# Kernel tuning notes

Measured on AMD Instinct MI355X. Metric: run time of the kernel, lower is better.

Reference implementation:

```python
import jax, jax.numpy as jnp
import numpy as np

N = 50000        # number of nodes
E = 1600000      # number of (directed) edges, ~degree 32
D = 128          # latent_dim
L = 2            # num_layers
NEG_SLOPE = 0.01 # torch F.leaky_relu default


def setup_inputs() -> dict:
    key = jax.random.key(0)
    k1, k2, k3, k4 = jax.random.split(key, 4)
    h = jax.random.normal(k1, (N, D), dtype=jnp.float32)
    src = jax.random.randint(k2, (E,), 0, N, dtype=jnp.int32)
    dst = jax.random.randint(k3, (E,), 0, N, dtype=jnp.int32)
    # attn_fc per layer: Linear(2*D, 1, bias=False) -> weight vector of length 2*D
    att_w = jax.random.normal(k4, (L, 2 * D), dtype=jnp.float32) * 0.1
    return {"h": h, "src": src, "dst": dst, "att_w": att_w}


def _segment_softmax(e, seg, n):
    # numerically-stable softmax over edges grouped by destination node
    m = jax.ops.segment_max(e, seg, num_segments=n)      # [N]
    ex = jnp.exp(e - m[seg])                             # [E]
    s = jax.ops.segment_sum(ex, seg, num_segments=n)     # [N]
    return ex / s[seg]


def reference(h, src, dst, att_w):
    n, d = h.shape
    for l in range(att_w.shape[0]):
        w_src = att_w[l, :d]   # weight applied to edges.src['h']
        w_dst = att_w[l, d:]   # weight applied to edges.dst['h']
        # a = attn_fc(concat(h_src, h_dst)) = h_src @ w_src + h_dst @ w_dst
        a = h[src] @ w_src + h[dst] @ w_dst               # [E]
        e = jnp.where(a > 0, a, NEG_SLOPE * a)            # leaky_relu
        alpha = _segment_softmax(e, dst, n)               # edge_softmax by dst
        # update_all: m = h_src * e ; h_dst = sum(m)
        h = jax.ops.segment_sum(h[src] * alpha[:, None], dst, num_segments=n)
    return h
```

## Files before the change

### kernel.cpp

```cpp
#include <hip/hip_runtime.h>
#include <hip/hip_fp16.h>
#include <math.h>

#define NEG_SLOPE 0.01f
#define BKT_BITS 7
#define BKT_MASK 127
#define SBLOCKS  256
#define STPB     512


__global__ void bkhist_kernel(const int* __restrict__ dst, int* __restrict__ blockhist,
                              int E, int NB, int chunk) {
    extern __shared__ int lh[];
    for (int k = threadIdx.x; k < NB; k += blockDim.x) lh[k] = 0;
    __syncthreads();
    int b = blockIdx.x;
    int beg = b * chunk, end = min(E, beg + chunk);
    for (int e = beg + (int)threadIdx.x; e < end; e += blockDim.x)
        atomicAdd(&lh[dst[e] >> BKT_BITS], 1);
    __syncthreads();
    for (int k = threadIdx.x; k < NB; k += blockDim.x)
        blockhist[k * SBLOCKS + b] = lh[k];
}

__global__ void scan1_kernel(const int* __restrict__ in, int* __restrict__ local_excl,
                             int* __restrict__ partials, int n) {
    __shared__ int sm[1024];
    int i = blockIdx.x * 1024 + threadIdx.x;
    int x = (i < n) ? in[i] : 0;
    sm[threadIdx.x] = x;
    __syncthreads();
    for (int off = 1; off < 1024; off <<= 1) {
        int y = (threadIdx.x >= (unsigned)off) ? sm[threadIdx.x - off] : 0;
        __syncthreads();
        sm[threadIdx.x] += y;
        __syncthreads();
    }
    if (i < n) local_excl[i] = sm[threadIdx.x] - x;
    if (threadIdx.x == 1023) partials[blockIdx.x] = sm[1023];
}

__global__ void scan2_kernel(int* __restrict__ partials, int nchunks) {
    __shared__ int sm[1024];
    int x = (threadIdx.x < (unsigned)nchunks) ? partials[threadIdx.x] : 0;
    sm[threadIdx.x] = x;
    __syncthreads();
    for (int off = 1; off < 1024; off <<= 1) {
        int y = (threadIdx.x >= (unsigned)off) ? sm[threadIdx.x - off] : 0;
        __syncthreads();
        sm[threadIdx.x] += y;
        __syncthreads();
    }
    partials[threadIdx.x] = sm[threadIdx.x] - x;
    if (threadIdx.x == 1023) partials[1024] = sm[1023];
}

__device__ __forceinline__ int bh_at(const int* __restrict__ local_ex,
                                     const int* __restrict__ partials, int i) {
    return local_ex[i] + partials[i >> 10];
}

__global__ void bksplit_kernel(const int* __restrict__ src, const int* __restrict__ dst,
                               const int* __restrict__ local_ex, const int* __restrict__ partials,
                               unsigned* __restrict__ pairs,
                               int E, int NB, int chunk) {
    extern __shared__ int lm[];
    int* lbase = lm;
    int* lcnt  = lm + NB;
    int b = blockIdx.x;
    for (int k = threadIdx.x; k < NB; k += blockDim.x) {
        lbase[k] = bh_at(local_ex, partials, k * SBLOCKS + b);
        lcnt[k]  = 0;
    }
    __syncthreads();
    int beg = b * chunk, end = min(E, beg + chunk);
    for (int e = beg + (int)threadIdx.x; e < end; e += blockDim.x) {
        int d = dst[e];
        int k = d >> BKT_BITS;
        int pos = lbase[k] + atomicAdd(&lcnt[k], 1);
        pairs[pos] = ((unsigned)src[e] << BKT_BITS) | (unsigned)(d & BKT_MASK);
    }
}

__global__ void csr_build_kernel(const unsigned* __restrict__ pairs,
                                 const int* __restrict__ local_ex, const int* __restrict__ partials,
                                 int* __restrict__ row_ptr, int* __restrict__ csr_src,
                                 int E, int N, int NB) {
    __shared__ int ldeg[128];
    __shared__ int lscan[128];
    __shared__ int lpos[128];
    int k = blockIdx.x;
    int bbase = bh_at(local_ex, partials, k * SBLOCKS);
    int bend  = (k == NB - 1) ? E : bh_at(local_ex, partials, (k + 1) * SBLOCKS);
    if (threadIdx.x < 128) ldeg[threadIdx.x] = 0;
    __syncthreads();
    for (int i = bbase + (int)threadIdx.x; i < bend; i += blockDim.x)
        atomicAdd(&ldeg[pairs[i] & BKT_MASK], 1);
    __syncthreads();
    int x = (threadIdx.x < 128) ? ldeg[threadIdx.x] : 0;
    if (threadIdx.x < 128) lscan[threadIdx.x] = x;
    __syncthreads();
    for (int off = 1; off < 128; off <<= 1) {
        int y = 0;
        if (threadIdx.x < 128 && threadIdx.x >= (unsigned)off) y = lscan[threadIdx.x - off];
        __syncthreads();
        if (threadIdx.x < 128) lscan[threadIdx.x] += y;
        __syncthreads();
    }
    if (threadIdx.x < 128) {
        int excl = lscan[threadIdx.x] - x;
        int node = (k << BKT_BITS) + threadIdx.x;
        if (node < N) row_ptr[node] = bbase + excl;
        lpos[threadIdx.x] = excl;
    }
    if (k == NB - 1 && threadIdx.x == 0) row_ptr[N] = E;
    __syncthreads();
    for (int i = bbase + (int)threadIdx.x; i < bend; i += blockDim.x) {
        unsigned p = pairs[i];
        int pos = atomicAdd(&lpos[p & BKT_MASK], 1);
        csr_src[bbase + pos] = (int)(p >> BKT_BITS);
    }
}


__global__ void stconv_kernel(const float* __restrict__ h, const float* __restrict__ att_w_l,
                              float* __restrict__ s, float* __restrict__ t,
                              __half* __restrict__ h16, int n) {
    int gid  = blockIdx.x * blockDim.x + threadIdx.x;
    int wid  = gid >> 6;
    int lane = threadIdx.x & 63;
    int half = lane >> 5;
    int hl   = lane & 31;
    int v    = wid * 2 + half;
    if (v >= n) return;
    float4 hv = ((const float4*)(h + (size_t)v * 128))[hl];
    __half2 p01 = __floats2half2_rn(hv.x, hv.y);
    __half2 p23 = __floats2half2_rn(hv.z, hv.w);
    float2 packed;
    packed.x = *(const float*)&p01;
    packed.y = *(const float*)&p23;
    ((float2*)(h16 + (size_t)v * 128))[hl] = packed;
    float4 ws = ((const float4*)att_w_l)[hl];
    float4 wd = ((const float4*)(att_w_l + 128))[hl];
    float ps = hv.x * ws.x + hv.y * ws.y + hv.z * ws.z + hv.w * ws.w;
    float pt = hv.x * wd.x + hv.y * wd.y + hv.z * wd.z + hv.w * wd.w;
    for (int off = 16; off > 0; off >>= 1) {
        ps += __shfl_down(ps, off);
        pt += __shfl_down(pt, off);
    }
    if (hl == 0) { s[v] = ps; t[v] = pt; }
}

__device__ __forceinline__ void gath8(const __half* __restrict__ hin, int u, float w,
                                      int qlane, float acc[8]) {
    float4 r = ((const float4*)(hin + ((size_t)(unsigned)u << 7)))[qlane];
    const __half2* hp = (const __half2*)&r;
    #pragma unroll
    for (int d = 0; d < 4; ++d) {
        acc[2 * d]     = fmaf(__low2float(hp[d]),  w, acc[2 * d]);
        acc[2 * d + 1] = fmaf(__high2float(hp[d]), w, acc[2 * d + 1]);
    }
}

template<bool LAST>
__global__ __launch_bounds__(256, 8)
void agg_kernel(const __half* __restrict__ hin, const float* __restrict__ s,
                const float* __restrict__ t, const int* __restrict__ row_ptr,
                const int* __restrict__ csr_src,
                __half* __restrict__ hout16, float* __restrict__ outf,
                const float* __restrict__ att_w_next,
                float* __restrict__ s2, float* __restrict__ t2, int n) {
    int gid   = blockIdx.x * blockDim.x + threadIdx.x;
    int v     = gid >> 6;
    int lane  = threadIdx.x & 63;
    if (v >= n) return;
    int quad  = lane >> 4;
    int qlane = lane & 15;

    int beg = row_ptr[v];
    int end = row_ptr[v + 1];
    float tv = t[v];

    float acc[8] = {0.f, 0.f, 0.f, 0.f, 0.f, 0.f, 0.f, 0.f};
    float lsum_l = 0.f;

    for (int base = beg; base < end; base += 64) {
        int cnt = end - base;
        if (cnt > 64) cnt = 64;
        int idx = base + min(lane, cnt - 1);
        int u   = csr_src[idx];
        float a = s[u] + tv;
        float e = (a > 0.f) ? a : NEG_SLOPE * a;
        float wl = (lane < cnt) ? __expf(e) : 0.f;
        lsum_l += wl;
        int steps = (cnt + 3) >> 2;
        int k = 0;
        for (; k + 3 < steps; k += 4) {
            int sl0 = (k << 2) + quad;
            int   u0 = __shfl(u, sl0);       float w0 = __shfl(wl, sl0);
            int   u1 = __shfl(u, sl0 + 4);   float w1 = __shfl(wl, sl0 + 4);
            int   u2 = __shfl(u, sl0 + 8);   float w2 = __shfl(wl, sl0 + 8);
            int   u3 = __shfl(u, sl0 + 12);  float w3 = __shfl(wl, sl0 + 12);
            gath8(hin, u0, w0, qlane, acc);
            gath8(hin, u1, w1, qlane, acc);
            gath8(hin, u2, w2, qlane, acc);
            gath8(hin, u3, w3, qlane, acc);
        }
        for (; k < steps; ++k) {
            int sl = (k << 2) + quad;
            int   u0 = __shfl(u, sl);
            float w0 = __shfl(wl, sl);
            gath8(hin, u0, w0, qlane, acc);
        }
    }
    #pragma unroll
    for (int j = 0; j < 8; ++j) {
        acc[j] += __shfl_xor(acc[j], 16);
        acc[j] += __shfl_xor(acc[j], 32);
    }
    float lsum = lsum_l;
    for (int off = 32; off > 0; off >>= 1) lsum += __shfl_xor(lsum, off);
    float inv_l = (lsum > 0.f) ? (1.0f / lsum) : 0.f;
    #pragma unroll
    for (int j = 0; j < 8; ++j) acc[j] *= inv_l;

    if (LAST) {
        if (quad == 0) {
            float4* op = (float4*)(outf + (size_t)v * 128);
            op[2 * qlane]     = make_float4(acc[0], acc[1], acc[2], acc[3]);
            op[2 * qlane + 1] = make_float4(acc[4], acc[5], acc[6], acc[7]);
        }
    } else {
        if (quad == 0) {
            __half2 p0 = __floats2half2_rn(acc[0], acc[1]);
            __half2 p1 = __floats2half2_rn(acc[2], acc[3]);
            __half2 p2 = __floats2half2_rn(acc[4], acc[5]);
            __half2 p3 = __floats2half2_rn(acc[6], acc[7]);
            int4 pk;
            pk.x = *(const int*)&p0; pk.y = *(const int*)&p1;
            pk.z = *(const int*)&p2; pk.w = *(const int*)&p3;
            ((int4*)(hout16 + (size_t)v * 128))[qlane] = pk;
        }
        float4 ws0 = ((const float4*)att_w_next)[2 * qlane];
        float4 ws1 = ((const float4*)att_w_next)[2 * qlane + 1];
        float4 wd0 = ((const float4*)(att_w_next + 128))[2 * qlane];
        float4 wd1 = ((const float4*)(att_w_next + 128))[2 * qlane + 1];
        float ps = acc[0] * ws0.x + acc[1] * ws0.y + acc[2] * ws0.z + acc[3] * ws0.w
                 + acc[4] * ws1.x + acc[5] * ws1.y + acc[6] * ws1.z + acc[7] * ws1.w;
        float pt = acc[0] * wd0.x + acc[1] * wd0.y + acc[2] * wd0.z + acc[3] * wd0.w
                 + acc[4] * wd1.x + acc[5] * wd1.y + acc[6] * wd1.z + acc[7] * wd1.w;
        for (int off = 8; off > 0; off >>= 1) {
            ps += __shfl_down(ps, off);
            pt += __shfl_down(pt, off);
        }
        if (lane == 0) { s2[v] = ps; t2[v] = pt; }
    }
}


extern "C" void kernel_launch(void* const* d_in, const int* in_sizes, int n_in,
                              void* d_out, int out_size, void* d_ws, size_t ws_size,
                              hipStream_t stream) {
    const float* h0    = (const float*)d_in[0];
    const int*   src   = (const int*)d_in[1];
    const int*   dst   = (const int*)d_in[2];
    const float* att_w = (const float*)d_in[3];
    int N = in_sizes[0] / 128;
    int E = in_sizes[1];
    int L = in_sizes[3] / 256;
    float* out = (float*)d_out;

    int NB = (N + BKT_MASK) >> BKT_BITS;
    int n2 = NB * SBLOCKS;
    int chunk = (E + SBLOCKS - 1) / SBLOCKS;
    int nch2 = (n2 + 1023) / 1024;

    char* ws = (char*)d_ws;
    size_t off = 0;
    auto alloc = [&](size_t bytes) -> void* {
        void* p = ws + off;
        off = (off + bytes + 511) & ~(size_t)511;
        return p;
    };
    int*      row_ptr   = (int*)     alloc((size_t)(N + 1) * 4);
    int*      csr_src   = (int*)     alloc((size_t)E * 4);
    float*    s1        = (float*)   alloc((size_t)N * 4);
    float*    t1        = (float*)   alloc((size_t)N * 4);
    float*    s2        = (float*)   alloc((size_t)N * 4);
    float*    t2        = (float*)   alloc((size_t)N * 4);
    __half*   hA        = (__half*)  alloc((size_t)N * 128 * 2);
    __half*   hB        = (__half*)  alloc((size_t)N * 128 * 2);
    unsigned* pairs     = (unsigned*)alloc((size_t)E * 4);
    int*      blockhist = (int*)     alloc((size_t)n2 * 4);
    int*      local_ex  = (int*)     alloc((size_t)n2 * 4);
    int*      partials  = (int*)     alloc(1025 * 4);

    bkhist_kernel<<<SBLOCKS, STPB, NB * 4, stream>>>(dst, blockhist, E, NB, chunk);
    scan1_kernel<<<nch2, 1024, 0, stream>>>(blockhist, local_ex, partials, n2);
    scan2_kernel<<<1, 1024, 0, stream>>>(partials, nch2);
    bksplit_kernel<<<SBLOCKS, STPB, 2 * NB * 4, stream>>>(src, dst, local_ex, partials,
                                                          pairs, E, NB, chunk);
    csr_build_kernel<<<NB, 512, 0, stream>>>(pairs, local_ex, partials,
                                             row_ptr, csr_src, E, N, NB);

    const int tb = 256;
    int node_blocks = (N * 64 + tb - 1) / tb;
    int st_blocks   = ((N + 1) / 2 * 64 + tb - 1) / tb;

    stconv_kernel<<<st_blocks, tb, 0, stream>>>(h0, att_w, s1, t1, hA, N);

    __half* hin = hA;
    __half* hnx = hB;
    float *sc = s1, *tc = t1, *sn = s2, *tn = t2;
    for (int l = 0; l < L; ++l) {
        if (l == L - 1) {
            agg_kernel<true><<<node_blocks, tb, 0, stream>>>(
                hin, sc, tc, row_ptr, csr_src, nullptr, out, nullptr, nullptr, nullptr, N);
        } else {
            agg_kernel<false><<<node_blocks, tb, 0, stream>>>(
                hin, sc, tc, row_ptr, csr_src, hnx, nullptr,
                att_w + (size_t)(l + 1) * 256, sn, tn, N);
            __half* tmp = hin; hin = hnx; hnx = tmp;
            float* tf;
            tf = sc; sc = sn; sn = tf;
            tf = tc; tc = tn; tn = tf;
        }
    }
}
```

Baseline: 222.0 us.

## Replace bucketed two-pass CSR build with global atomic degree histogram and scatter

Swaps the bucket-sort CSR construction (per-block bucket histograms, bucket split into a pairs buffer, per-bucket local sort) for a direct scheme. It builds a global per-node degree histogram with atomics, scans it, then scatters each source into its slot with an atomicSub on the degree counter. The aggregation kernel now computes row offsets from the scan output and partials instead of a separate row_ptr array. This removes the pairs buffer and one pass over the edges, at the cost of heavy contention on global atomics and uncoalesced scattered writes. Neighbor order within a row also becomes nondeterministic, which changes floating-point summation order.

```diff
diff --git a/kernel.cpp b/kernel.cpp
--- a/kernel.cpp
+++ b/kernel.cpp
@@ -3,24 +3,12 @@
 #include <math.h>
 
 #define NEG_SLOPE 0.01f
-#define BKT_BITS 7
-#define BKT_MASK 127
-#define SBLOCKS  256
-#define STPB     512
-
-
-__global__ void bkhist_kernel(const int* __restrict__ dst, int* __restrict__ blockhist,
-                              int E, int NB, int chunk) {
-    extern __shared__ int lh[];
-    for (int k = threadIdx.x; k < NB; k += blockDim.x) lh[k] = 0;
-    __syncthreads();
-    int b = blockIdx.x;
-    int beg = b * chunk, end = min(E, beg + chunk);
-    for (int e = beg + (int)threadIdx.x; e < end; e += blockDim.x)
-        atomicAdd(&lh[dst[e] >> BKT_BITS], 1);
-    __syncthreads();
-    for (int k = threadIdx.x; k < NB; k += blockDim.x)
-        blockhist[k * SBLOCKS + b] = lh[k];
+
+
+__global__ void deghist_kernel(const int* __restrict__ dst, int* __restrict__ deg, int E) {
+    int stride = gridDim.x * blockDim.x;
+    for (int e = blockIdx.x * blockDim.x + threadIdx.x; e < E; e += stride)
+        atomicAdd(&deg[dst[e]], 1);
 }
 
 __global__ void scan1_kernel(const int* __restrict__ in, int* __restrict__ local_excl,
@@ -55,70 +43,15 @@
     if (threadIdx.x == 1023) partials[1024] = sm[1023];
 }
 
-__device__ __forceinline__ int bh_at(const int* __restrict__ local_ex,
-                                     const int* __restrict__ partials, int i) {
-    return local_ex[i] + partials[i >> 10];
-}
-
-__global__ void bksplit_kernel(const int* __restrict__ src, const int* __restrict__ dst,
-                               const int* __restrict__ local_ex, const int* __restrict__ partials,
-                               unsigned* __restrict__ pairs,
-                               int E, int NB, int chunk) {
-    extern __shared__ int lm[];
-    int* lbase = lm;
-    int* lcnt  = lm + NB;
-    int b = blockIdx.x;
-    for (int k = threadIdx.x; k < NB; k += blockDim.x) {
-        lbase[k] = bh_at(local_ex, partials, k * SBLOCKS + b);
-        lcnt[k]  = 0;
-    }
-    __syncthreads();
-    int beg = b * chunk, end = min(E, beg + chunk);
-    for (int e = beg + (int)threadIdx.x; e < end; e += blockDim.x) {
+__global__ void scatter_kernel(const int* __restrict__ src, const int* __restrict__ dst,
+                               const int* __restrict__ lex, const int* __restrict__ par,
+                               int* __restrict__ deg, int* __restrict__ csr_src, int E) {
+    int stride = gridDim.x * blockDim.x;
+    for (int e = blockIdx.x * blockDim.x + threadIdx.x; e < E; e += stride) {
         int d = dst[e];
-        int k = d >> BKT_BITS;
-        int pos = lbase[k] + atomicAdd(&lcnt[k], 1);
-        pairs[pos] = ((unsigned)src[e] << BKT_BITS) | (unsigned)(d & BKT_MASK);
-    }
-}
-
-__global__ void csr_build_kernel(const unsigned* __restrict__ pairs,
-                                 const int* __restrict__ local_ex, const int* __restrict__ partials,
-                                 int* __restrict__ row_ptr, int* __restrict__ csr_src,
-                                 int E, int N, int NB) {
-    __shared__ int ldeg[128];
-    __shared__ int lscan[128];
-    __shared__ int lpos[128];
-    int k = blockIdx.x;
-    int bbase = bh_at(local_ex, partials, k * SBLOCKS);
-    int bend  = (k == NB - 1) ? E : bh_at(local_ex, partials, (k + 1) * SBLOCKS);
-    if (threadIdx.x < 128) ldeg[threadIdx.x] = 0;
-    __syncthreads();
-    for (int i = bbase + (int)threadIdx.x; i < bend; i += blockDim.x)
-        atomicAdd(&ldeg[pairs[i] & BKT_MASK], 1);
-    __syncthreads();
-    int x = (threadIdx.x < 128) ? ldeg[threadIdx.x] : 0;
-    if (threadIdx.x < 128) lscan[threadIdx.x] = x;
-    __syncthreads();
-    for (int off = 1; off < 128; off <<= 1) {
-        int y = 0;
-        if (threadIdx.x < 128 && threadIdx.x >= (unsigned)off) y = lscan[threadIdx.x - off];
-        __syncthreads();
-        if (threadIdx.x < 128) lscan[threadIdx.x] += y;
-        __syncthreads();
-    }
-    if (threadIdx.x < 128) {
-        int excl = lscan[threadIdx.x] - x;
-        int node = (k << BKT_BITS) + threadIdx.x;
-        if (node < N) row_ptr[node] = bbase + excl;
-        lpos[threadIdx.x] = excl;
-    }
-    if (k == NB - 1 && threadIdx.x == 0) row_ptr[N] = E;
-    __syncthreads();
-    for (int i = bbase + (int)threadIdx.x; i < bend; i += blockDim.x) {
-        unsigned p = pairs[i];
-        int pos = atomicAdd(&lpos[p & BKT_MASK], 1);
-        csr_src[bbase + pos] = (int)(p >> BKT_BITS);
+        int slot = atomicSub(&deg[d], 1) - 1;
+        int base = lex[d] + par[d >> 10];
+        csr_src[base + slot] = src[e];
     }
 }
 
@@ -165,8 +98,8 @@
 template<bool LAST>
 __global__ __launch_bounds__(256, 8)
 void agg_kernel(const __half* __restrict__ hin, const float* __restrict__ s,
-                const float* __restrict__ t, const int* __restrict__ row_ptr,
-                const int* __restrict__ csr_src,
+                const float* __restrict__ t, const int* __restrict__ lex,
+                const int* __restrict__ par, const int* __restrict__ csr_src,
                 __half* __restrict__ hout16, float* __restrict__ outf,
                 const float* __restrict__ att_w_next,
                 float* __restrict__ s2, float* __restrict__ t2, int n) {
@@ -177,8 +110,8 @@
     int quad  = lane >> 4;
     int qlane = lane & 15;
 
-    int beg = row_ptr[v];
-    int end = row_ptr[v + 1];
+    int beg = lex[v]     + par[v >> 10];
+    int end = lex[v + 1] + par[(v + 1) >> 10];
     float tv = t[v];
 
     float acc[8] = {0.f, 0.f, 0.f, 0.f, 0.f, 0.f, 0.f, 0.f};
@@ -270,10 +203,8 @@
     int L = in_sizes[3] / 256;
     float* out = (float*)d_out;
 
-    int NB = (N + BKT_MASK) >> BKT_BITS;
-    int n2 = NB * SBLOCKS;
-    int chunk = (E + SBLOCKS - 1) / SBLOCKS;
-    int nch2 = (n2 + 1023) / 1024;
+    int n1 = N + 1;
+    int nch = (n1 + 1023) / 1024;
 
     char* ws = (char*)d_ws;
     size_t off = 0;
@@ -282,26 +213,22 @@
         off = (off + bytes + 511) & ~(size_t)511;
         return p;
     };
-    int*      row_ptr   = (int*)     alloc((size_t)(N + 1) * 4);
     int*      csr_src   = (int*)     alloc((size_t)E * 4);
+    int*      deg       = (int*)     alloc((size_t)n1 * 4);
+    int*      local_ex  = (int*)     alloc((size_t)n1 * 4);
+    int*      partials  = (int*)     alloc(1025 * 4);
     float*    s1        = (float*)   alloc((size_t)N * 4);
     float*    t1        = (float*)   alloc((size_t)N * 4);
     float*    s2        = (float*)   alloc((size_t)N * 4);
     float*    t2        = (float*)   alloc((size_t)N * 4);
     __half*   hA        = (__half*)  alloc((size_t)N * 128 * 2);
     __half*   hB        = (__half*)  alloc((size_t)N * 128 * 2);
-    unsigned* pairs     = (unsigned*)alloc((size_t)E * 4);
-    int*      blockhist = (int*)     alloc((size_t)n2 * 4);
-    int*      local_ex  = (int*)     alloc((size_t)n2 * 4);
-    int*      partials  = (int*)     alloc(1025 * 4);
-
-    bkhist_kernel<<<SBLOCKS, STPB, NB * 4, stream>>>(dst, blockhist, E, NB, chunk);
-    scan1_kernel<<<nch2, 1024, 0, stream>>>(blockhist, local_ex, partials, n2);
-    scan2_kernel<<<1, 1024, 0, stream>>>(partials, nch2);
-    bksplit_kernel<<<SBLOCKS, STPB, 2 * NB * 4, stream>>>(src, dst, local_ex, partials,
-                                                          pairs, E, NB, chunk);
-    csr_build_kernel<<<NB, 512, 0, stream>>>(pairs, local_ex, partials,
-                                             row_ptr, csr_src, E, N, NB);
+
+    hipMemsetAsync(deg, 0, (size_t)n1 * 4, stream);
+    deghist_kernel<<<2048, 256, 0, stream>>>(dst, deg, E);
+    scan1_kernel<<<nch, 1024, 0, stream>>>(deg, local_ex, partials, n1);
+    scan2_kernel<<<1, 1024, 0, stream>>>(partials, nch);
+    scatter_kernel<<<2048, 256, 0, stream>>>(src, dst, local_ex, partials, deg, csr_src, E);
 
     const int tb = 256;
     int node_blocks = (N * 64 + tb - 1) / tb;
@@ -315,11 +242,12 @@
     for (int l = 0; l < L; ++l) {
         if (l == L - 1) {
             agg_kernel<true><<<node_blocks, tb, 0, stream>>>(
-                hin, sc, tc, row_ptr, csr_src, nullptr, out, nullptr, nullptr, nullptr, N);
+                hin, sc, tc, local_ex, partials, csr_src,
+                nullptr, out, nullptr, nullptr, nullptr, N);
         } else {
             agg_kernel<false><<<node_blocks, tb, 0, stream>>>(
-                hin, sc, tc, row_ptr, csr_src, hnx, nullptr,
-                att_w + (size_t)(l + 1) * 256, sn, tn, N);
+                hin, sc, tc, local_ex, partials, csr_src,
+                hnx, nullptr, att_w + (size_t)(l + 1) * 256, sn, tn, N);
             __half* tmp = hin; hin = hnx; hnx = tmp;
             float* tf;
             tf = sc; sc = sn; sn = tf;
```

Measured after the change: 343.2 us. 1.55x slower.
